# Optimization experiments

Measured on AMD Instinct MI355X. Metric: run time of the kernel, lower is better.

Reference implementation:

```python
import jax, jax.numpy as jnp
import numpy as np

B, S, T = 64, 512, 256  # batch, seq_len, num_tags


def setup_inputs() -> dict:
    key = jax.random.key(0)
    k1, k2, k3, k4 = jax.random.split(key, 4)
    emissions = jax.random.normal(k1, (B, S, T), dtype=jnp.float32)
    tags = jax.random.randint(k2, (B, S), 0, T, dtype=jnp.int32)
    mask = jnp.ones((B, S), dtype=bool)
    # nn.init.uniform_(-0.01, 0.01) as in reset_parameters()
    transitions = jax.random.uniform(k3, (T, T), minval=-0.01, maxval=0.01, dtype=jnp.float32)
    tse = jax.random.uniform(k4, (T + 2, T + 2), minval=-0.01, maxval=0.01, dtype=jnp.float32)
    tse = tse.at[T + 1, T].set(-10000.0)  # transitions[end_tag, start_tag] = -10000
    return {"emissions": emissions, "tags": tags, "mask": mask,
            "transitions": transitions, "transitions_with_start_end": tse}


def reference(emissions, tags, mask, transitions, transitions_with_start_end):
    Bv, Sv, Tv = emissions.shape
    start, end = Tv, Tv + 1

    # ---- forward algorithm (log partition), faithful to the torch recurrence:
    # new[b, j] = alpha[b, j] + logsumexp_k( trans[k, j] + emit_t[b, k] )
    # (the mask line fv*mask + fv*~mask in the original is a no-op)
    alpha0 = emissions[:, 0] + transitions_with_start_end[start, :Tv]

    def step(alpha, em_t):  # em_t: [B, T]
        lse = jax.nn.logsumexp(transitions[None, :, :] + em_t[:, :, None], axis=1)  # [B, T]
        return alpha + lse, None

    ems = jnp.swapaxes(emissions[:, 1:], 0, 1)  # [S-1, B, T]
    alpha, _ = jax.lax.scan(step, alpha0, ems)
    forward_score = jax.nn.logsumexp(alpha + transitions_with_start_end[:Tv, end], axis=1)  # [B]

    # ---- gold path score
    mf = mask.astype(emissions.dtype)
    emit = jnp.take_along_axis(emissions, tags[:, :, None].astype(jnp.int32), axis=2)[:, :, 0]  # [B, S]
    score = transitions_with_start_end[start, tags[:, 0]]
    score = score + jnp.sum(emit * mf, axis=1)
    score = score + jnp.sum(transitions[tags[:, 1:], tags[:, :-1]] * mf[:, 1:], axis=1)
    last_idx = jnp.sum(mask.astype(jnp.int32), axis=1) - 1  # [B]
    last_tags = jnp.take_along_axis(tags, last_idx[:, None], axis=1)[:, 0]
    score = score + transitions_with_start_end[last_tags, end]

    return forward_score - score  # negative log-likelihood per batch element, [B]
```

## Files before the change

kernel.cpp:

```cpp
#include <hip/hip_runtime.h>
#include <cstdint>

#define B_ 64
#define S_ 512
#define T_ 256
#define TP2 258

#define BM 32

typedef __attribute__((ext_vector_type(8))) short short8;
typedef __attribute__((ext_vector_type(4))) float f32x4;

__device__ __forceinline__ ushort f2bf(float f) {
    union { float f; uint32_t u; } c; c.f = f;
    uint32_t u = c.u;
    u += 0x7FFFu + ((u >> 16) & 1u);
    return (ushort)(u >> 16);
}

__global__ void prep_w(const float* __restrict__ trans, ushort* __restrict__ wt,
                       float* __restrict__ accb) {
    int k = blockIdx.x;
    int n = threadIdx.x;
    wt[n * T_ + k] = f2bf(__expf(trans[k * T_ + n]));
    if (k < B_) accb[k * T_ + n] = 0.f;
}

__global__ __launch_bounds__(256, 4) void gemm_lse(
    const float* __restrict__ em, const ushort* __restrict__ wt,
    float* __restrict__ accb)
{
    __shared__ alignas(16) ushort Afrag[8 * 2 * 512];

    int blk   = blockIdx.x;
    long r0   = (long)blk * BM;
    int batch = blk >> 4;
    bool has_s0 = (blk & 15) == 0;

    int tid  = threadIdx.x;
    int wv   = tid >> 6;
    int lane = tid & 63;
    int quad = lane >> 4;
    int l15  = lane & 15;
    int n0   = wv * 64;

    #pragma unroll
    for (int q = 0; q < 4; ++q) {
        int s   = tid + q * 256;
        int row = s >> 5;
        int kq  = s & 31;
        const float* src = em + (r0 + row) * T_ + kq * 8;
        float4 va = *(const float4*)(src);
        float4 vb = *(const float4*)(src + 4);
        union { ushort u[8]; uint4 v; } pk;
        pk.u[0] = f2bf(__expf(va.x)); pk.u[1] = f2bf(__expf(va.y));
        pk.u[2] = f2bf(__expf(va.z)); pk.u[3] = f2bf(__expf(va.w));
        pk.u[4] = f2bf(__expf(vb.x)); pk.u[5] = f2bf(__expf(vb.y));
        pk.u[6] = f2bf(__expf(vb.z)); pk.u[7] = f2bf(__expf(vb.w));
        int kt = kq >> 2, qd = kq & 3, ih = row >> 4, rl = row & 15;
        *(uint4*)&Afrag[kt * 1024 + ih * 512 + (qd * 16 + rl) * 8] = pk.v;
    }
    __syncthreads();

    f32x4 acc[2][4];
    #pragma unroll
    for (int i = 0; i < 2; ++i)
        #pragma unroll
        for (int j = 0; j < 4; ++j)
            acc[i][j] = (f32x4){0.f, 0.f, 0.f, 0.f};

    for (int kt = 0; kt < 8; ++kt) {
        short8 af0 = *(const short8*)&Afrag[kt * 1024 + lane * 8];
        short8 af1 = *(const short8*)&Afrag[kt * 1024 + 512 + lane * 8];
        #pragma unroll
        for (int j = 0; j < 4; ++j) {
            short8 bf = *(const short8*)&wt[(n0 + j * 16 + l15) * T_ + kt * 32 + quad * 8];
            acc[0][j] = __builtin_amdgcn_mfma_f32_16x16x32_bf16(af0, bf, acc[0][j], 0, 0, 0);
            acc[1][j] = __builtin_amdgcn_mfma_f32_16x16x32_bf16(af1, bf, acc[1][j], 0, 0, 0);
        }
    }

    #pragma unroll
    for (int j = 0; j < 4; ++j) {
        float s = 0.f;
        #pragma unroll
        for (int i = 0; i < 2; ++i) {
            f32x4 a = acc[i][j];
            #pragma unroll
            for (int v = 0; v < 4; ++v) {
                bool skip = has_s0 && (i == 0) && (quad == 0) && (v == 0);
                if (!skip) s += __logf(a[v]);
            }
        }
        s += __shfl_xor(s, 16);
        s += __shfl_xor(s, 32);
        if (lane < 16)
            atomicAdd(&accb[batch * T_ + n0 + j * 16 + lane], s);
    }
}

__global__ __launch_bounds__(256) void finalize(
    const float* __restrict__ em, const int* __restrict__ tags,
    const float* __restrict__ trans, const float* __restrict__ tse,
    const float* __restrict__ accb, float* __restrict__ out)
{
    __shared__ float red[8];
    int b = blockIdx.x;
    int j = threadIdx.x;
    int w = j >> 6;

    float v = em[(long)b * S_ * T_ + j] + tse[T_ * TP2 + j]
            + accb[b * T_ + j] + tse[j * TP2 + (T_ + 1)];

    float m = v;
    #pragma unroll
    for (int o = 32; o; o >>= 1) m = fmaxf(m, __shfl_xor(m, o));
    if ((j & 63) == 0) red[w] = m;
    __syncthreads();
    m = fmaxf(fmaxf(red[0], red[1]), fmaxf(red[2], red[3]));

    float e = __expf(v - m);
    #pragma unroll
    for (int o = 32; o; o >>= 1) e += __shfl_xor(e, o);
    if ((j & 63) == 0) red[4 + w] = e;
    __syncthreads();
    float fwd = m + __logf(red[4] + red[5] + red[6] + red[7]);

    const int* tg = tags + b * S_;
    float sc = 0.f;
    for (int s = j; s < S_; s += 256) {
        int t = tg[s];
        sc += em[((long)b * S_ + s) * T_ + t];
        if (s >= 1) sc += trans[t * T_ + tg[s - 1]];
    }
    if (j == 0) {
        sc += tse[T_ * TP2 + tg[0]];
        sc += tse[tg[S_ - 1] * TP2 + (T_ + 1)];
    }
    #pragma unroll
    for (int o = 32; o; o >>= 1) sc += __shfl_xor(sc, o);
    __syncthreads();
    if ((j & 63) == 0) red[w] = sc;
    __syncthreads();
    if (j == 0) out[b] = fwd - (red[0] + red[1] + red[2] + red[3]);
}

extern "C" void kernel_launch(void* const* d_in, const int* in_sizes, int n_in,
                              void* d_out, int out_size, void* d_ws, size_t ws_size,
                              hipStream_t stream) {
    const float* em    = (const float*)d_in[0];
    const int*   tags  = (const int*)d_in[1];
    const float* trans = (const float*)d_in[3];
    const float* tse   = (const float*)d_in[4];
    float* out = (float*)d_out;

    ushort* wt   = (ushort*)d_ws;
    float*  accb = (float*)((char*)d_ws + 131072);

    prep_w<<<T_, T_, 0, stream>>>(trans, wt, accb);
    gemm_lse<<<(B_ * S_) / BM, 256, 0, stream>>>(em, wt, accb);
    finalize<<<B_, T_, 0, stream>>>(em, tags, trans, tse, accb, out);
}
```

Measured before the change: 101.0 us.

## Give each wave a 16-row tile over all columns, drop LDS staging and atomics

```diff
diff --git a/kernel.cpp b/kernel.cpp
--- a/kernel.cpp
+++ b/kernel.cpp
@@ -5,8 +5,6 @@
 #define S_ 512
 #define T_ 256
 #define TP2 258
-
-#define BM 32
 
 typedef __attribute__((ext_vector_type(8))) short short8;
 typedef __attribute__((ext_vector_type(4))) float f32x4;
@@ -18,99 +16,101 @@
     return (ushort)(u >> 16);
 }
 
-__global__ void prep_w(const float* __restrict__ trans, ushort* __restrict__ wt,
-                       float* __restrict__ accb) {
+__global__ void prep_w(const float* __restrict__ trans, ushort* __restrict__ wt) {
     int k = blockIdx.x;
     int n = threadIdx.x;
     wt[n * T_ + k] = f2bf(__expf(trans[k * T_ + n]));
-    if (k < B_) accb[k * T_ + n] = 0.f;
 }
 
-__global__ __launch_bounds__(256, 4) void gemm_lse(
+__global__ __launch_bounds__(256, 2) void gemm_lse(
     const float* __restrict__ em, const ushort* __restrict__ wt,
-    float* __restrict__ accb)
+    float* __restrict__ accP)
 {
-    __shared__ alignas(16) ushort Afrag[8 * 2 * 512];
-
-    int blk   = blockIdx.x;
-    long r0   = (long)blk * BM;
-    int batch = blk >> 4;
-    bool has_s0 = (blk & 15) == 0;
-
     int tid  = threadIdx.x;
     int wv   = tid >> 6;
     int lane = tid & 63;
     int quad = lane >> 4;
     int l15  = lane & 15;
-    int n0   = wv * 64;
 
+    int wgl  = blockIdx.x * 4 + wv;
+    long r0  = (long)wgl * 16;
+    bool has_s0 = (r0 & (S_ - 1)) == 0;
+
+    const float* ap = em + (r0 + l15) * T_ + quad * 8;
+
+    float4 va = *(const float4*)(ap);
+    float4 vb = *(const float4*)(ap + 4);
+
+    f32x4 acc[16];
     #pragma unroll
-    for (int q = 0; q < 4; ++q) {
-        int s   = tid + q * 256;
-        int row = s >> 5;
-        int kq  = s & 31;
-        const float* src = em + (r0 + row) * T_ + kq * 8;
-        float4 va = *(const float4*)(src);
-        float4 vb = *(const float4*)(src + 4);
-        union { ushort u[8]; uint4 v; } pk;
-        pk.u[0] = f2bf(__expf(va.x)); pk.u[1] = f2bf(__expf(va.y));
-        pk.u[2] = f2bf(__expf(va.z)); pk.u[3] = f2bf(__expf(va.w));
-        pk.u[4] = f2bf(__expf(vb.x)); pk.u[5] = f2bf(__expf(vb.y));
-        pk.u[6] = f2bf(__expf(vb.z)); pk.u[7] = f2bf(__expf(vb.w));
-        int kt = kq >> 2, qd = kq & 3, ih = row >> 4, rl = row & 15;
-        *(uint4*)&Afrag[kt * 1024 + ih * 512 + (qd * 16 + rl) * 8] = pk.v;
-    }
-    __syncthreads();
-
-    f32x4 acc[2][4];
-    #pragma unroll
-    for (int i = 0; i < 2; ++i)
-        #pragma unroll
-        for (int j = 0; j < 4; ++j)
-            acc[i][j] = (f32x4){0.f, 0.f, 0.f, 0.f};
+    for (int j = 0; j < 16; ++j) acc[j] = (f32x4){0.f, 0.f, 0.f, 0.f};
 
     for (int kt = 0; kt < 8; ++kt) {
-        short8 af0 = *(const short8*)&Afrag[kt * 1024 + lane * 8];
-        short8 af1 = *(const short8*)&Afrag[kt * 1024 + 512 + lane * 8];
+        short8 bf0[8];
         #pragma unroll
-        for (int j = 0; j < 4; ++j) {
-            short8 bf = *(const short8*)&wt[(n0 + j * 16 + l15) * T_ + kt * 32 + quad * 8];
-            acc[0][j] = __builtin_amdgcn_mfma_f32_16x16x32_bf16(af0, bf, acc[0][j], 0, 0, 0);
-            acc[1][j] = __builtin_amdgcn_mfma_f32_16x16x32_bf16(af1, bf, acc[1][j], 0, 0, 0);
+        for (int j = 0; j < 8; ++j)
+            bf0[j] = *(const short8*)&wt[(j * 16 + l15) * T_ + kt * 32 + quad * 8];
+
+        float4 na = va, nb = vb;
+        if (kt < 7) {
+            na = *(const float4*)(ap + (kt + 1) * 32);
+            nb = *(const float4*)(ap + (kt + 1) * 32 + 4);
         }
+
+        union { ushort u[8]; short8 v; } af;
+        af.u[0] = f2bf(__expf(va.x)); af.u[1] = f2bf(__expf(va.y));
+        af.u[2] = f2bf(__expf(va.z)); af.u[3] = f2bf(__expf(va.w));
+        af.u[4] = f2bf(__expf(vb.x)); af.u[5] = f2bf(__expf(vb.y));
+        af.u[6] = f2bf(__expf(vb.z)); af.u[7] = f2bf(__expf(vb.w));
+
+        #pragma unroll
+        for (int j = 0; j < 8; ++j)
+            acc[j] = __builtin_amdgcn_mfma_f32_16x16x32_bf16(af.v, bf0[j], acc[j], 0, 0, 0);
+
+        short8 bf1[8];
+        #pragma unroll
+        for (int j = 0; j < 8; ++j)
+            bf1[j] = *(const short8*)&wt[((j + 8) * 16 + l15) * T_ + kt * 32 + quad * 8];
+        #pragma unroll
+        for (int j = 0; j < 8; ++j)
+            acc[8 + j] = __builtin_amdgcn_mfma_f32_16x16x32_bf16(af.v, bf1[j], acc[8 + j], 0, 0, 0);
+
+        va = na; vb = nb;
     }
 
     #pragma unroll
-    for (int j = 0; j < 4; ++j) {
+    for (int j = 0; j < 16; ++j) {
         float s = 0.f;
+        f32x4 a = acc[j];
         #pragma unroll
-        for (int i = 0; i < 2; ++i) {
-            f32x4 a = acc[i][j];
-            #pragma unroll
-            for (int v = 0; v < 4; ++v) {
-                bool skip = has_s0 && (i == 0) && (quad == 0) && (v == 0);
-                if (!skip) s += __logf(a[v]);
-            }
+        for (int v = 0; v < 4; ++v) {
+            bool skip = has_s0 && (quad == 0) && (v == 0);
+            if (!skip) s += __logf(a[v]);
         }
         s += __shfl_xor(s, 16);
         s += __shfl_xor(s, 32);
         if (lane < 16)
-            atomicAdd(&accb[batch * T_ + n0 + j * 16 + lane], s);
+            accP[wgl * T_ + j * 16 + lane] = s;
     }
 }
 
 __global__ __launch_bounds__(256) void finalize(
     const float* __restrict__ em, const int* __restrict__ tags,
     const float* __restrict__ trans, const float* __restrict__ tse,
-    const float* __restrict__ accb, float* __restrict__ out)
+    const float* __restrict__ accP, float* __restrict__ out)
 {
     __shared__ float red[8];
     int b = blockIdx.x;
     int j = threadIdx.x;
     int w = j >> 6;
 
+    float p = 0.f;
+    #pragma unroll
+    for (int q = 0; q < 32; ++q)
+        p += accP[(b * 32 + q) * T_ + j];
+
     float v = em[(long)b * S_ * T_ + j] + tse[T_ * TP2 + j]
-            + accb[b * T_ + j] + tse[j * TP2 + (T_ + 1)];
+            + p + tse[j * TP2 + (T_ + 1)];
 
     float m = v;
     #pragma unroll
@@ -155,9 +155,9 @@
     float* out = (float*)d_out;
 
     ushort* wt   = (ushort*)d_ws;
-    float*  accb = (float*)((char*)d_ws + 131072);
+    float*  accP = (float*)((char*)d_ws + 131072);
 
-    prep_w<<<T_, T_, 0, stream>>>(trans, wt, accb);
-    gemm_lse<<<(B_ * S_) / BM, 256, 0, stream>>>(em, wt, accb);
-    finalize<<<B_, T_, 0, stream>>>(em, tags, trans, tse, accb, out);
+    prep_w<<<T_, T_, 0, stream>>>(trans, wt);
+    gemm_lse<<<512, 256, 0, stream>>>(em, wt, accP);
+    finalize<<<B_, T_, 0, stream>>>(em, tags, trans, tse, accP, out);
 }
```

New measurement: 117.6 us. +16.5%, slower.
